# Kernel optimization log

Hardware: AMD Instinct MI355X
Metric: run time of the kernel (lower is better)

The kernel has to match this reference:

```python
import jax, jax.numpy as jnp
import numpy as np
from math import factorial

IRREPS = [0] * 256 + [1] * 256 + [2] * 128 + [3] * 64
N_BATCH, CHANNELS = 1024, 32


def _dfact(n):
    r = 1
    while n > 1:
        r *= n
        n -= 2
    return r


def _sh_l(l, xyz):
    """Real spherical harmonics of degree l, components m=-l..l, at unit vectors xyz."""
    x, y, z = xyz[:, 0], xyz[:, 1], xyz[:, 2]
    phi = np.arctan2(y, x)
    ct = z
    st = np.sqrt(np.clip(1.0 - ct * ct, 0.0, None))
    Y = np.zeros((xyz.shape[0], 2 * l + 1))
    for m in range(l + 1):
        pmm = ((-1.0) ** m) * _dfact(2 * m - 1) * st ** m  # P_m^m(cos t)
        if l == m:
            plm = pmm
        else:
            pm1 = ct * (2 * m + 1) * pmm  # P_{m+1}^m
            if l == m + 1:
                plm = pm1
            else:
                p2, p1 = pmm, pm1
                for ll in range(m + 2, l + 1):
                    p2, p1 = p1, ((2 * ll - 1) * ct * p1 - (ll + m - 1) * p2) / (ll - m)
                plm = p1
        K = np.sqrt((2 * l + 1) / (4 * np.pi) * factorial(l - m) / factorial(l + m))
        if m == 0:
            Y[:, l] = K * plm
        else:
            Y[:, l + m] = np.sqrt(2.0) * K * np.cos(m * phi) * plm
            Y[:, l - m] = np.sqrt(2.0) * K * np.sin(m * phi) * plm
    return Y


def _j_matrix(l):
    """Orthogonal involution J_l: real-SH matrix of the y<->z axis swap (J = J^T = J^-1)."""
    rng = np.random.default_rng(0)
    v = rng.normal(size=(max(256, 16 * (2 * l + 1)), 3))
    v /= np.linalg.norm(v, axis=1, keepdims=True)
    A = _sh_l(l, v)
    B = _sh_l(l, v[:, [0, 2, 1]])  # Y(swap r)
    X, _, _, _ = np.linalg.lstsq(A, B, rcond=None)
    return X.T  # Y(swap r) = J @ Y(r)


def _build_info():
    freq, rev, groups = [], [], []
    off = 0
    i = 0
    while i < len(IRREPS):
        l = IRREPS[i]
        mul = 0
        while i < len(IRREPS) and IRREPS[i] == l:
            mul += 1
            i += 1
        d = 2 * l + 1
        groups.append((l, off, mul, np.asarray(_j_matrix(l), np.float32)))
        for _ in range(mul):
            for k in range(d):
                freq.append(k - l)      # m value of component k
                rev.append(off + (d - 1 - k))  # index of the -m partner
            off += d
    return np.asarray(freq, np.float32), np.asarray(rev, np.int32), groups, off


FREQ_NP, REV_NP, GROUPS, DIM = _build_info()
FREQ = jnp.asarray(FREQ_NP)
REV = jnp.asarray(REV_NP)
J_MATS = [jnp.asarray(J) for (_, _, _, J) in GROUPS]


def _z_rot(x, theta):
    """Per-m z-rotation (sparse vecsca): out_m = cos(m t) x_m - sin(m t) x_{-m}."""
    ang = theta[:, None] * FREQ  # (N, DIM)
    return jnp.cos(ang)[..., None] * x - jnp.sin(ang)[..., None] * x[:, REV, :]


def _j_apply(x):
    """Block-diagonal J application, grouped by l (sparse scale / flip stage)."""
    n, _, c = x.shape
    outs = []
    for (l, off, mul, _), J in zip(GROUPS, J_MATS):
        d = 2 * l + 1
        seg = x[:, off:off + mul * d, :].reshape(n, mul, d, c)
        outs.append(jnp.einsum('pq,nmqc->nmpc', J, seg).reshape(n, mul * d, c))
    return jnp.concatenate(outs, axis=1)


def setup_inputs() -> dict:
    key = jax.random.key(0)
    k0, k1, k2, k3 = jax.random.split(key, 4)
    two_pi = 2.0 * np.pi
    return {
        'input': jax.random.normal(k0, (N_BATCH, DIM, CHANNELS), dtype=jnp.float32),
        'alpha': jax.random.uniform(k1, (N_BATCH,), dtype=jnp.float32) * two_pi,
        'beta': jax.random.uniform(k2, (N_BATCH,), dtype=jnp.float32) * two_pi,
        'gamma': jax.random.uniform(k3, (N_BATCH,), dtype=jnp.float32) * two_pi,
    }


def reference(input, alpha, beta, gamma):
    # D(alpha, beta, gamma) = Dz(alpha) J Dz(beta) J Dz(gamma)
    x = _z_rot(input, gamma)
    x = _j_apply(x)
    x = _z_rot(x, beta)
    x = _j_apply(x)
    return _z_rot(x, alpha)
```

## Files before the change

### kernel.cpp

```cpp
#include <hip/hip_runtime.h>
#include <math.h>


namespace {

typedef float f4 __attribute__((ext_vector_type(4)));

constexpr float SQ3_2 = 0.86602540378443864676f;
constexpr float S6    = 0.61237243569579452455f;
constexpr float S10   = 0.79056941504209483300f;
constexpr float S15   = 0.96824583655185422129f;

template<int L> struct JM;
template<> struct JM<1> {
  static constexpr float v[3][3] = {
    { 0.f, -1.f, 0.f},
    {-1.f,  0.f, 0.f},
    { 0.f,  0.f, 1.f}};
};
template<> struct JM<2> {
  static constexpr float v[5][5] = {
    { 0.f, 0.f,  0.f,   -1.f,  0.f},
    { 0.f, 1.f,  0.f,    0.f,  0.f},
    { 0.f, 0.f, -0.5f,   0.f, -SQ3_2},
    {-1.f, 0.f,  0.f,    0.f,  0.f},
    { 0.f, 0.f, -SQ3_2,  0.f,  0.5f}};
};
template<> struct JM<3> {
  static constexpr float v[7][7] = {
    { 0.f, 0.f, 0.f, S10,  0.f,   -S6,  0.f},
    { 0.f, 1.f, 0.f, 0.f,  0.f,    0.f, 0.f},
    { 0.f, 0.f, 0.f, S6,   0.f,    S10, 0.f},
    { S10, 0.f, S6,  0.f,  0.f,    0.f, 0.f},
    { 0.f, 0.f, 0.f, 0.f, -0.25f,  0.f, -S15},
    {-S6,  0.f, S10, 0.f,  0.f,    0.f, 0.f},
    { 0.f, 0.f, 0.f, 0.f, -S15,    0.f, 0.25f}};
};

template<int L>
__device__ inline void compute_M_col(int q, float al, float be, float ga, float* M) {
  constexpr int D = 2 * L + 1;
  const int mq = q - L;
  float sg, cg;
  sincosf((float)mq * ga, &sg, &cg);
  float v[D];
#pragma unroll
  for (int p = 0; p < D; ++p)
    v[p] = cg * JM<L>::v[p][q] + sg * JM<L>::v[p][(D - 1) - q];
  float c1, s1;
  sincosf(be, &s1, &c1);
  float cb[L + 1], sb[L + 1];
  cb[0] = 1.f; sb[0] = 0.f;
  cb[1] = c1;  sb[1] = s1;
#pragma unroll
  for (int k = 2; k <= L; ++k) {
    cb[k] = 2.f * c1 * cb[k - 1] - cb[k - 2];
    sb[k] = 2.f * c1 * sb[k - 1] - sb[k - 2];
  }
  float w[D];
#pragma unroll
  for (int p = 0; p < D; ++p) {
    const int mp = p - L;
    const int am = mp < 0 ? -mp : mp;
    const float c = cb[am];
    const float s = mp < 0 ? -sb[am] : sb[am];
    w[p] = c * v[p] - s * v[(D - 1) - p];
  }
  float u[D];
#pragma unroll
  for (int p = 0; p < D; ++p) {
    float acc = 0.f;
#pragma unroll
    for (int r = 0; r < D; ++r) acc = fmaf(JM<L>::v[p][r], w[r], acc);
    u[p] = acc;
  }
  sincosf(al, &s1, &c1);
  float ca[L + 1], sa[L + 1];
  ca[0] = 1.f; sa[0] = 0.f;
  ca[1] = c1;  sa[1] = s1;
#pragma unroll
  for (int k = 2; k <= L; ++k) {
    ca[k] = 2.f * c1 * ca[k - 1] - ca[k - 2];
    sa[k] = 2.f * c1 * sa[k - 1] - sa[k - 2];
  }
#pragma unroll
  for (int p = 0; p < D; ++p) {
    const int mp = p - L;
    const int am = mp < 0 ? -mp : mp;
    const float c = ca[am];
    const float s = mp < 0 ? -sa[am] : sa[am];
    M[p * D + q] = c * u[p] - s * u[(D - 1) - p];
  }
}

__global__ __launch_bounds__(256) void build_M_kernel(
    const float* __restrict__ alpha, const float* __restrict__ beta,
    const float* __restrict__ gamma, float* __restrict__ ws, int n_batch) {
  const int t = threadIdx.x;
  const int n = blockIdx.x * 16 + (t >> 4);
  const int col = t & 15;
  if (n >= n_batch || col >= 15) return;
  const float al = alpha[n], be = beta[n], ga = gamma[n];
  float* w = ws + (size_t)n * 96;
  if (col < 7)       compute_M_col<3>(col,      al, be, ga, w);
  else if (col < 12) compute_M_col<2>(col - 7,  al, be, ga, w + 49);
  else               compute_M_col<1>(col - 12, al, be, ga, w + 74);
}

template<int D>
__device__ inline void apply_unit(const f4* __restrict__ inU,
                                  f4* __restrict__ outU,
                                  const float* __restrict__ M,
                                  int g, int ch) {
  const f4* src = inU + g * (D * 8) + ch;
  f4* dst = outU + g * (D * 8) + ch;
  f4 v[D];
#pragma unroll
  for (int q = 0; q < D; ++q) v[q] = __builtin_nontemporal_load(src + q * 8);
#pragma unroll
  for (int p = 0; p < D; ++p) {
    const float* Mrow = M + p * D;
    f4 a = Mrow[0] * v[0];
#pragma unroll
    for (int q = 1; q < D; ++q) a += Mrow[q] * v[q];
    __builtin_nontemporal_store(a, dst + p * 8);
  }
}

__global__ __launch_bounds__(512) void wigner_stream_kernel(
    const float* __restrict__ in, const float* __restrict__ ws,
    float* __restrict__ out, int n_units) {
  __shared__ float M[49];
  const int t = threadIdx.x;
  const int g = t >> 3, ch = t & 7;
  for (int u = blockIdx.x; u < n_units; u += 1023) {
    const int n = u >> 3, k = u & 7;
    const size_t base = (size_t)n * 16896;
    const f4* inN = (const f4*)in + base;
    f4* outN = (f4*)out + base;
    if (k == 0) {
#pragma unroll
      for (int j = 0; j < 4; ++j)
        __builtin_nontemporal_store(
            __builtin_nontemporal_load(inN + t + 512 * j), outN + t + 512 * j);
    } else {
      int D, moff, soff;
      if (k <= 4)      { D = 3; moff = 74; soff = 2048 + (k - 1) * 1536; }
      else if (k <= 6) { D = 5; moff = 49; soff = 8192 + (k - 5) * 2560; }
      else             { D = 7; moff = 0;  soff = 13312; }
      if (t < D * D) M[t] = ws[(size_t)n * 96 + moff + t];
      __syncthreads();
      if (k <= 4)      apply_unit<3>(inN + soff, outN + soff, M, g, ch);
      else if (k <= 6) apply_unit<5>(inN + soff, outN + soff, M, g, ch);
      else             apply_unit<7>(inN + soff, outN + soff, M, g, ch);
      __syncthreads();
    }
  }
}

}

extern "C" void kernel_launch(void* const* d_in, const int* in_sizes, int n_in,
                              void* d_out, int out_size, void* d_ws, size_t ws_size,
                              hipStream_t stream) {
  const float* in    = (const float*)d_in[0];
  const float* alpha = (const float*)d_in[1];
  const float* beta  = (const float*)d_in[2];
  const float* gamma = (const float*)d_in[3];
  float* out = (float*)d_out;
  const int n_batch = in_sizes[1];

  float* ws = (float*)d_ws;
  build_M_kernel<<<(n_batch + 15) / 16, 256, 0, stream>>>(alpha, beta, gamma,
                                                          ws, n_batch);
  const int n_units = n_batch * 8;
  const int grid = n_units < 1023 ? n_units : 1023;
  wigner_stream_kernel<<<grid, 512, 0, stream>>>(in, ws, out, n_units);
}
```

Before: 113.0 us.

## Load Wigner matrices into scalar registers and regroup work units

Each work unit now reads its small rotation matrix straight from global memory through readfirstlane loads into registers, replacing the shared-memory staging and both block barriers. Blocks shrink to 256 threads and each thread handles several irrep copies (4 for l=1, 2 for l=2/3), with all loads issued before the stores. The batch is split into 6 units instead of 8 and the grid is resized to match. This should give more memory-level parallelism and less sync overhead, at the cost of higher register pressure per thread.

```diff
diff --git a/kernel.cpp b/kernel.cpp
--- a/kernel.cpp
+++ b/kernel.cpp
@@ -107,53 +107,77 @@
   else               compute_M_col<1>(col - 12, al, be, ga, w + 74);
 }
 
-template<int D>
+__device__ inline float uload(const float* __restrict__ p) {
+  return __int_as_float(__builtin_amdgcn_readfirstlane(__float_as_int(*p)));
+}
+
+template<int D, int NC>
 __device__ inline void apply_unit(const f4* __restrict__ inU,
                                   f4* __restrict__ outU,
-                                  const float* __restrict__ M,
+                                  const float* __restrict__ Ms,
                                   int g, int ch) {
-  const f4* src = inU + g * (D * 8) + ch;
-  f4* dst = outU + g * (D * 8) + ch;
-  f4 v[D];
-#pragma unroll
-  for (int q = 0; q < D; ++q) v[q] = __builtin_nontemporal_load(src + q * 8);
-#pragma unroll
-  for (int p = 0; p < D; ++p) {
-    const float* Mrow = M + p * D;
-    f4 a = Mrow[0] * v[0];
-#pragma unroll
-    for (int q = 1; q < D; ++q) a += Mrow[q] * v[q];
-    __builtin_nontemporal_store(a, dst + p * 8);
-  }
-}
-
-__global__ __launch_bounds__(512) void wigner_stream_kernel(
+  const int base = g * (NC * D * 8) + ch;
+  f4 v[NC][D];
+#pragma unroll
+  for (int j = 0; j < NC; ++j)
+#pragma unroll
+    for (int q = 0; q < D; ++q)
+      v[j][q] = __builtin_nontemporal_load(inU + base + (j * D + q) * 8);
+  f4 o[NC][D];
+#pragma unroll
+  for (int j = 0; j < NC; ++j)
+#pragma unroll
+    for (int p = 0; p < D; ++p) {
+      f4 a = Ms[p * D] * v[j][0];
+#pragma unroll
+      for (int q = 1; q < D; ++q) a += Ms[p * D + q] * v[j][q];
+      o[j][p] = a;
+    }
+#pragma unroll
+  for (int j = 0; j < NC; ++j)
+#pragma unroll
+    for (int p = 0; p < D; ++p)
+      __builtin_nontemporal_store(o[j][p], outU + base + (j * D + p) * 8);
+}
+
+template<int D>
+__device__ inline void run_unit(const f4* __restrict__ inU, f4* __restrict__ outU,
+                                const float* __restrict__ ws_n, int moff,
+                                int g, int ch) {
+  float Ms[D * D];
+#pragma unroll
+  for (int i = 0; i < D * D; ++i) Ms[i] = uload(ws_n + moff + i);
+  constexpr int NC = (D == 3) ? 4 : 2;
+  apply_unit<D, NC>(inU, outU, Ms, g, ch);
+}
+
+__global__ __launch_bounds__(256) void wigner_stream_kernel(
     const float* __restrict__ in, const float* __restrict__ ws,
-    float* __restrict__ out, int n_units) {
-  __shared__ float M[49];
+    float* __restrict__ out, int n_units, int grid) {
   const int t = threadIdx.x;
   const int g = t >> 3, ch = t & 7;
-  for (int u = blockIdx.x; u < n_units; u += 1023) {
-    const int n = u >> 3, k = u & 7;
+  for (int u = blockIdx.x; u < n_units; u += grid) {
+    const int n = u / 6, k = u - n * 6;
     const size_t base = (size_t)n * 16896;
     const f4* inN = (const f4*)in + base;
     f4* outN = (f4*)out + base;
+    const float* ws_n = ws + (size_t)n * 96;
     if (k == 0) {
-#pragma unroll
-      for (int j = 0; j < 4; ++j)
-        __builtin_nontemporal_store(
-            __builtin_nontemporal_load(inN + t + 512 * j), outN + t + 512 * j);
+      f4 c[8];
+#pragma unroll
+      for (int j = 0; j < 8; ++j)
+        c[j] = __builtin_nontemporal_load(inN + t + 256 * j);
+#pragma unroll
+      for (int j = 0; j < 8; ++j)
+        __builtin_nontemporal_store(c[j], outN + t + 256 * j);
+    } else if (k <= 2) {
+      const int soff = 2048 + (k - 1) * 3072;
+      run_unit<3>(inN + soff, outN + soff, ws_n, 74, g, ch);
+    } else if (k <= 4) {
+      const int soff = 8192 + (k - 3) * 2560;
+      run_unit<5>(inN + soff, outN + soff, ws_n, 49, g, ch);
     } else {
-      int D, moff, soff;
-      if (k <= 4)      { D = 3; moff = 74; soff = 2048 + (k - 1) * 1536; }
-      else if (k <= 6) { D = 5; moff = 49; soff = 8192 + (k - 5) * 2560; }
-      else             { D = 7; moff = 0;  soff = 13312; }
-      if (t < D * D) M[t] = ws[(size_t)n * 96 + moff + t];
-      __syncthreads();
-      if (k <= 4)      apply_unit<3>(inN + soff, outN + soff, M, g, ch);
-      else if (k <= 6) apply_unit<5>(inN + soff, outN + soff, M, g, ch);
-      else             apply_unit<7>(inN + soff, outN + soff, M, g, ch);
-      __syncthreads();
+      run_unit<7>(inN + 13312, outN + 13312, ws_n, 0, g, ch);
     }
   }
 }
@@ -173,7 +197,7 @@
   float* ws = (float*)d_ws;
   build_M_kernel<<<(n_batch + 15) / 16, 256, 0, stream>>>(alpha, beta, gamma,
                                                           ws, n_batch);
-  const int n_units = n_batch * 8;
-  const int grid = n_units < 1023 ? n_units : 1023;
-  wigner_stream_kernel<<<grid, 512, 0, stream>>>(in, ws, out, n_units);
-}
+  const int n_units = n_batch * 6;
+  const int grid = n_units < 1025 ? n_units : 1025;
+  wigner_stream_kernel<<<grid, 256, 0, stream>>>(in, ws, out, n_units, grid);
+}
```

Result: faster. 108.2 us (-4.3%).
